# Optimization experiments

Measured on AMD Instinct MI355X. Metric: run time of the kernel, lower is better.

Reference implementation:

```python
import jax, jax.numpy as jnp
import numpy as np

N = 100000  # nodes
E = 600000  # edges
D = 128     # input_dim
H = D // 2  # hidden of MLP head
OUT = 10    # output_dim
EPS = 1e-5
NEG_SLOPE = 0.2


def _p(key, shape, scale):
    return jax.random.normal(key, shape, dtype=jnp.float32) * scale


def setup_inputs() -> dict:
    key = jax.random.key(0)
    ks = jax.random.split(key, 16)
    s = 1.0 / np.sqrt(D)
    return {
        "x": jax.random.normal(ks[0], (N, D), dtype=jnp.float32),
        "edge_index": jax.random.randint(ks[1], (2, E), 0, N, dtype=jnp.int64),
        # SAGEConv: lin_l (applied to mean-aggregated neighbors, has bias), lin_r (root)
        "sage_Wl": _p(ks[2], (D, D), s), "sage_Wr": _p(ks[3], (D, D), s),
        "sage_b": jnp.zeros((D,), jnp.float32),
        # GCNConv
        "gcn_W": _p(ks[4], (D, D), s), "gcn_b": jnp.zeros((D,), jnp.float32),
        # GATConv (heads=1)
        "gat_W": _p(ks[5], (D, D), s),
        "gat_att_src": _p(ks[6], (D,), s), "gat_att_dst": _p(ks[7], (D,), s),
        "gat_b": jnp.zeros((D,), jnp.float32),
        # BatchNorms (batch-stat normalization)
        "bn1_g": jnp.ones((D,), jnp.float32), "bn1_b": jnp.zeros((D,), jnp.float32),
        "bn2_g": jnp.ones((D,), jnp.float32), "bn2_b": jnp.zeros((D,), jnp.float32),
        "bn3_g": jnp.ones((D,), jnp.float32), "bn3_b": jnp.zeros((D,), jnp.float32),
        # MLP head
        "lin1_W": _p(ks[8], (D, H), s), "lin1_b": jnp.zeros((H,), jnp.float32),
        "lin2_W": _p(ks[9], (H, OUT), 1.0 / np.sqrt(H)), "lin2_b": jnp.zeros((OUT,), jnp.float32),
    }


def _bn_relu(x, g, b):
    mu = jnp.mean(x, axis=0)
    var = jnp.mean(jnp.square(x - mu), axis=0)
    return jax.nn.relu((x - mu) * jax.lax.rsqrt(var + EPS) * g + b)


def _sage(x, src, dst, Wl, Wr, b):
    agg = jax.ops.segment_sum(x[src], dst, num_segments=N)          # [N, D]
    cnt = jax.ops.segment_sum(jnp.ones((src.shape[0],), x.dtype), dst, num_segments=N)
    mean = agg / jnp.maximum(cnt, 1.0)[:, None]
    return mean @ Wl + x @ Wr + b


def _gcn(x, src, dst, W, b):
    loop = jnp.arange(N, dtype=src.dtype)
    s = jnp.concatenate([src, loop]); d = jnp.concatenate([dst, loop])
    deg = jax.ops.segment_sum(jnp.ones((d.shape[0],), x.dtype), d, num_segments=N)
    dinv = jnp.where(deg > 0, jax.lax.rsqrt(jnp.maximum(deg, 1.0)), 0.0)
    xw = x @ W
    msg = xw[s] * (dinv[s] * dinv[d])[:, None]
    return jax.ops.segment_sum(msg, d, num_segments=N) + b


def _gat(x, src, dst, W, att_s, att_d, b):
    loop = jnp.arange(N, dtype=src.dtype)
    s = jnp.concatenate([src, loop]); d = jnp.concatenate([dst, loop])
    xw = x @ W                                  # [N, D]
    a_s = xw @ att_s                            # [N]
    a_d = xw @ att_d                            # [N]
    e = jax.nn.leaky_relu(a_s[s] + a_d[d], NEG_SLOPE)  # [E+N]
    m = jax.ops.segment_max(e, d, num_segments=N)
    ee = jnp.exp(e - m[d])
    z = jax.ops.segment_sum(ee, d, num_segments=N)
    alpha = ee / z[d]
    return jax.ops.segment_sum(alpha[:, None] * xw[s], d, num_segments=N) + b


def reference(x, edge_index, sage_Wl, sage_Wr, sage_b, gcn_W, gcn_b,
              gat_W, gat_att_src, gat_att_dst, gat_b,
              bn1_g, bn1_b, bn2_g, bn2_b, bn3_g, bn3_b,
              lin1_W, lin1_b, lin2_W, lin2_b):
    src, dst = edge_index[0], edge_index[1]
    h = _bn_relu(_sage(x, src, dst, sage_Wl, sage_Wr, sage_b), bn1_g, bn1_b)
    h = _bn_relu(_gcn(h, src, dst, gcn_W, gcn_b), bn2_g, bn2_b)
    h = _bn_relu(_gat(h, src, dst, gat_W, gat_att_src, gat_att_dst, gat_b), bn3_g, bn3_b)
    # dropout is identity in eval mode
    h = jax.nn.relu(h @ lin1_W + lin1_b) @ lin2_W + lin2_b
    return jax.nn.log_softmax(h, axis=1)
```

## Files before the change

kernel.cpp:

```cpp
#include <hip/hip_runtime.h>

static constexpr int Dd = 128;
static constexpr int Hh = 64;
static constexpr int OC = 10;
#define CDIV(a,b) (((a)+(b)-1)/(b))

typedef __attribute__((ext_vector_type(8))) short short8v;
typedef __attribute__((ext_vector_type(16))) float f32x16;
typedef unsigned short u16;

__device__ __forceinline__ float lrelu(float x){ return x>0.f? x : 0.2f*x; }
__device__ __forceinline__ unsigned f2bf(float f){
  unsigned u = __float_as_uint(f);
  return (u + 0x7FFFu + ((u>>16)&1u)) >> 16;
}
__device__ __forceinline__ float bl(unsigned u){ return __uint_as_float(u<<16); }
__device__ __forceinline__ float bh(unsigned u){ return __uint_as_float(u & 0xFFFF0000u); }
__device__ __forceinline__ int swz(int byte, int row){ return byte ^ ((row&7)<<4); }

__global__ __launch_bounds__(256) void k_hist(const int* __restrict__ dst, int E,
    int* __restrict__ cnt) {
  int e = blockIdx.x*256 + threadIdx.x;
  if (e < E) atomicAdd(cnt + dst[e], 1);
}

__global__ __launch_bounds__(256) void k_scan_l1(const int* __restrict__ cnt,
    int* __restrict__ rp, int n, int* __restrict__ bsum) {
  __shared__ int sdata[256];
  int t = threadIdx.x;
  int base = blockIdx.x*2048 + t*8;
  int v[8]; int s = 0;
  #pragma unroll
  for (int k = 0; k < 8; k++) { v[k] = (base+k < n) ? cnt[base+k] : 0; s += v[k]; }
  sdata[t] = s; __syncthreads();
  for (int off = 1; off < 256; off <<= 1) {
    int a = sdata[t];
    int b = (t >= off) ? sdata[t-off] : 0;
    __syncthreads();
    sdata[t] = a + b;
    __syncthreads();
  }
  int ex = sdata[t] - s;
  if (t == 255) bsum[blockIdx.x] = sdata[255];
  int run = ex;
  #pragma unroll
  for (int k = 0; k < 8; k++) { if (base+k < n) rp[base+k] = run; run += v[k]; }
}

__global__ void k_scan_l2(int* __restrict__ bsum, int nb) {
  if (threadIdx.x == 0 && blockIdx.x == 0) {
    int run = 0;
    for (int i = 0; i < nb; i++) { int v = bsum[i]; bsum[i] = run; run += v; }
  }
}

__global__ __launch_bounds__(256) void k_scan_l3(int* __restrict__ rp, int n,
    const int* __restrict__ bsum, int E) {
  int off = bsum[blockIdx.x];
  int base = blockIdx.x*2048 + threadIdx.x*8;
  #pragma unroll
  for (int k = 0; k < 8; k++) if (base+k < n) rp[base+k] += off;
  if (blockIdx.x == 0 && threadIdx.x == 0) rp[n] = E;
}

__global__ __launch_bounds__(256) void k_fill(const int* __restrict__ src,
    const int* __restrict__ dst, int E, const int* __restrict__ rp,
    int* __restrict__ cnt, int* __restrict__ col) {
  int e = blockIdx.x*256 + threadIdx.x;
  if (e >= E) return;
  int d = dst[e];
  int pos = rp[d] + atomicSub(cnt + d, 1) - 1;
  col[pos] = src[e];
}

__global__ __launch_bounds__(256) void k_wt(const float* __restrict__ W,
    u16* __restrict__ WT, int K, int N) {
  int idx = blockIdx.x*256 + threadIdx.x;
  if (idx >= K*N) return;
  int n = idx / K, k = idx % K;
  WT[idx] = (u16)f2bf(W[k*N + n]);
}

__global__ __launch_bounds__(256) void k_tobf16(const float* __restrict__ in,
    u16* __restrict__ out, int n8) {
  int idx = blockIdx.x*256 + threadIdx.x;
  if (idx >= n8) return;
  const float4* p = reinterpret_cast<const float4*>(in) + idx*2;
  float4 v0 = p[0], v1 = p[1];
  uint4 w;
  w.x = f2bf(v0.x) | (f2bf(v0.y)<<16);
  w.y = f2bf(v0.z) | (f2bf(v0.w)<<16);
  w.z = f2bf(v1.x) | (f2bf(v1.y)<<16);
  w.w = f2bf(v1.z) | (f2bf(v1.w)<<16);
  reinterpret_cast<uint4*>(out)[idx] = w;
}

__global__ __launch_bounds__(256) void k_sage_gather(const u16* __restrict__ xb,
    const int* __restrict__ rp, const int* __restrict__ col,
    u16* __restrict__ ob, int n) {
  int gid = blockIdx.x*256 + threadIdx.x;
  int i = gid >> 5, l = gid & 31;
  if (i >= n) return;
  int beg = rp[i], end = rp[i+1];
  const u16* xp = xb + l*4;
  float a0=0.f, a1=0.f, a2=0.f, a3=0.f;
  int j = beg;
  for (; j+4 <= end; j += 4) {
    int s0=col[j], s1=col[j+1], s2=col[j+2], s3=col[j+3];
    uint2 v0 = *reinterpret_cast<const uint2*>(xp + (size_t)s0*Dd);
    uint2 v1 = *reinterpret_cast<const uint2*>(xp + (size_t)s1*Dd);
    uint2 v2 = *reinterpret_cast<const uint2*>(xp + (size_t)s2*Dd);
    uint2 v3 = *reinterpret_cast<const uint2*>(xp + (size_t)s3*Dd);
    a0 += (bl(v0.x)+bl(v1.x)) + (bl(v2.x)+bl(v3.x));
    a1 += (bh(v0.x)+bh(v1.x)) + (bh(v2.x)+bh(v3.x));
    a2 += (bl(v0.y)+bl(v1.y)) + (bl(v2.y)+bl(v3.y));
    a3 += (bh(v0.y)+bh(v1.y)) + (bh(v2.y)+bh(v3.y));
  }
  for (; j < end; j++) {
    int s = col[j];
    uint2 v = *reinterpret_cast<const uint2*>(xp + (size_t)s*Dd);
    a0 += bl(v.x); a1 += bh(v.x); a2 += bl(v.y); a3 += bh(v.y);
  }
  float inv = 1.0f / fmaxf((float)(end - beg), 1.0f);
  uint2 o;
  o.x = f2bf(a0*inv) | (f2bf(a1*inv)<<16);
  o.y = f2bf(a2*inv) | (f2bf(a3*inv)<<16);
  *reinterpret_cast<uint2*>(ob + (size_t)i*Dd + l*4) = o;
}

__global__ __launch_bounds__(256) void k_dinv(const int* __restrict__ rp,
    float* __restrict__ dinv, int n) {
  int i = blockIdx.x*256 + threadIdx.x;
  if (i < n) dinv[i] = rsqrtf((float)(rp[i+1] - rp[i]) + 1.0f);
}

__global__ __launch_bounds__(256) void k_gcn_gather(const u16* __restrict__ xb,
    const int* __restrict__ rp, const int* __restrict__ col,
    const float* __restrict__ dinv, u16* __restrict__ ob, int n) {
  int gid = blockIdx.x*256 + threadIdx.x;
  int i = gid >> 5, l = gid & 31;
  if (i >= n) return;
  int beg = rp[i], end = rp[i+1];
  const u16* xp = xb + l*4;
  float a0=0.f, a1=0.f, a2=0.f, a3=0.f;
  int j = beg;
  for (; j+4 <= end; j += 4) {
    int s0=col[j], s1=col[j+1], s2=col[j+2], s3=col[j+3];
    uint2 v0 = *reinterpret_cast<const uint2*>(xp + (size_t)s0*Dd);
    uint2 v1 = *reinterpret_cast<const uint2*>(xp + (size_t)s1*Dd);
    uint2 v2 = *reinterpret_cast<const uint2*>(xp + (size_t)s2*Dd);
    uint2 v3 = *reinterpret_cast<const uint2*>(xp + (size_t)s3*Dd);
    float w0 = dinv[s0], w1 = dinv[s1], w2 = dinv[s2], w3 = dinv[s3];
    a0 += (w0*bl(v0.x)+w1*bl(v1.x)) + (w2*bl(v2.x)+w3*bl(v3.x));
    a1 += (w0*bh(v0.x)+w1*bh(v1.x)) + (w2*bh(v2.x)+w3*bh(v3.x));
    a2 += (w0*bl(v0.y)+w1*bl(v1.y)) + (w2*bl(v2.y)+w3*bl(v3.y));
    a3 += (w0*bh(v0.y)+w1*bh(v1.y)) + (w2*bh(v2.y)+w3*bh(v3.y));
  }
  for (; j < end; j++) {
    int s = col[j];
    float w = dinv[s];
    uint2 v = *reinterpret_cast<const uint2*>(xp + (size_t)s*Dd);
    a0 += w*bl(v.x); a1 += w*bh(v.x); a2 += w*bl(v.y); a3 += w*bh(v.y);
  }
  float di = dinv[i];
  float ws = di*di;
  uint2 sv = *reinterpret_cast<const uint2*>(xp + (size_t)i*Dd);
  a0 = di*a0 + ws*bl(sv.x); a1 = di*a1 + ws*bh(sv.x);
  a2 = di*a2 + ws*bl(sv.y); a3 = di*a3 + ws*bh(sv.y);
  uint2 o;
  o.x = f2bf(a0) | (f2bf(a1)<<16);
  o.y = f2bf(a2) | (f2bf(a3)<<16);
  *reinterpret_cast<uint2*>(ob + (size_t)i*Dd + l*4) = o;
}

__global__ __launch_bounds__(256) void k_gat_gather(const u16* __restrict__ xb,
    const int* __restrict__ rp, const int* __restrict__ col,
    const float* __restrict__ a_s, const float* __restrict__ a_d,
    u16* __restrict__ ob, int n) {
  int gid = blockIdx.x*256 + threadIdx.x;
  int i = gid >> 5, l = gid & 31;
  if (i >= n) return;
  int beg = rp[i], end = rp[i+1];
  const u16* xp = xb + l*4;
  float ad = a_d[i];
  float es = lrelu(a_s[i] + ad);
  float m = es;
  int j = beg;
  for (; j+4 <= end; j += 4) {
    float e0 = lrelu(a_s[col[j]]   + ad);
    float e1 = lrelu(a_s[col[j+1]] + ad);
    float e2 = lrelu(a_s[col[j+2]] + ad);
    float e3 = lrelu(a_s[col[j+3]] + ad);
    m = fmaxf(m, fmaxf(fmaxf(e0,e1), fmaxf(e2,e3)));
  }
  for (; j < end; j++)
    m = fmaxf(m, lrelu(a_s[col[j]] + ad));
  float z = __expf(es - m);
  uint2 sv = *reinterpret_cast<const uint2*>(xp + (size_t)i*Dd);
  float a0 = z*bl(sv.x), a1 = z*bh(sv.x), a2 = z*bl(sv.y), a3 = z*bh(sv.y);
  j = beg;
  for (; j+4 <= end; j += 4) {
    int s0=col[j], s1=col[j+1], s2=col[j+2], s3=col[j+3];
    uint2 v0 = *reinterpret_cast<const uint2*>(xp + (size_t)s0*Dd);
    uint2 v1 = *reinterpret_cast<const uint2*>(xp + (size_t)s1*Dd);
    uint2 v2 = *reinterpret_cast<const uint2*>(xp + (size_t)s2*Dd);
    uint2 v3 = *reinterpret_cast<const uint2*>(xp + (size_t)s3*Dd);
    float w0 = __expf(lrelu(a_s[s0]+ad) - m);
    float w1 = __expf(lrelu(a_s[s1]+ad) - m);
    float w2 = __expf(lrelu(a_s[s2]+ad) - m);
    float w3 = __expf(lrelu(a_s[s3]+ad) - m);
    z += (w0+w1) + (w2+w3);
    a0 += (w0*bl(v0.x)+w1*bl(v1.x)) + (w2*bl(v2.x)+w3*bl(v3.x));
    a1 += (w0*bh(v0.x)+w1*bh(v1.x)) + (w2*bh(v2.x)+w3*bh(v3.x));
    a2 += (w0*bl(v0.y)+w1*bl(v1.y)) + (w2*bl(v2.y)+w3*bl(v3.y));
    a3 += (w0*bh(v0.y)+w1*bh(v1.y)) + (w2*bh(v2.y)+w3*bh(v3.y));
  }
  for (; j < end; j++) {
    int s = col[j];
    float w = __expf(lrelu(a_s[s]+ad) - m);
    z += w;
    uint2 v = *reinterpret_cast<const uint2*>(xp + (size_t)s*Dd);
    a0 += w*bl(v.x); a1 += w*bh(v.x); a2 += w*bl(v.y); a3 += w*bh(v.y);
  }
  float inv = 1.0f / z;
  uint2 o;
  o.x = f2bf(a0*inv) | (f2bf(a1*inv)<<16);
  o.y = f2bf(a2*inv) | (f2bf(a3*inv)<<16);
  *reinterpret_cast<uint2*>(ob + (size_t)i*Dd + l*4) = o;
}

__global__ __launch_bounds__(256) void k_bn_stats_bf(const u16* __restrict__ X, int M,
    float* __restrict__ gsum, float* __restrict__ gsq) {
  __shared__ float ss[2][256];
  int t = threadIdx.x;
  int cd = t & 63;
  int rg = t >> 6;
  float s0=0.f, q0=0.f, s1=0.f, q1=0.f;
  const unsigned* Xu = reinterpret_cast<const unsigned*>(X);
  for (int r = blockIdx.x*4 + rg; r < M; r += gridDim.x*4) {
    unsigned v = Xu[(size_t)r*64 + cd];
    float a = bl(v), b = bh(v);
    s0 += a; q0 += a*a; s1 += b; q1 += b*b;
  }
  ss[0][t] = s0; ss[1][t] = q0; __syncthreads();
  float rs0 = 0.f, rq0 = 0.f;
  if (rg == 0) {
    rs0 = ss[0][cd] + ss[0][cd+64] + ss[0][cd+128] + ss[0][cd+192];
    rq0 = ss[1][cd] + ss[1][cd+64] + ss[1][cd+128] + ss[1][cd+192];
  }
  __syncthreads();
  ss[0][t] = s1; ss[1][t] = q1; __syncthreads();
  if (rg == 0) {
    float rs1 = ss[0][cd] + ss[0][cd+64] + ss[0][cd+128] + ss[0][cd+192];
    float rq1 = ss[1][cd] + ss[1][cd+64] + ss[1][cd+128] + ss[1][cd+192];
    atomicAdd(gsum + 2*cd,     rs0); atomicAdd(gsq + 2*cd,     rq0);
    atomicAdd(gsum + 2*cd + 1, rs1); atomicAdd(gsq + 2*cd + 1, rq1);
  }
}

__global__ __launch_bounds__(128) void k_bn_final(const float* __restrict__ gsum,
    const float* __restrict__ gsq, int M, const float* __restrict__ g,
    const float* __restrict__ b, float* __restrict__ scale, float* __restrict__ shift) {
  int c = threadIdx.x;
  float mu = gsum[c] / (float)M;
  float var = fmaxf(gsq[c] / (float)M - mu*mu, 0.f);
  float sc = g[c] * rsqrtf(var + 1e-5f);
  scale[c] = sc;
  shift[c] = b[c] - mu*sc;
}

template<int NCOLS, bool DUAL, bool BNA, bool STATS, bool BIASRELU, bool ATT, bool OUTBF>
__global__ __launch_bounds__(256) void k_mm(
    const u16* __restrict__ A1, const u16* __restrict__ A2,
    const u16* __restrict__ WT1, const u16* __restrict__ WT2,
    const float* __restrict__ bnsc, const float* __restrict__ bnsh,
    const float* __restrict__ bias,
    void* __restrict__ Cout, int M,
    float* __restrict__ gsum, float* __restrict__ gsq,
    const float* __restrict__ att_sv, const float* __restrict__ att_dv,
    float* __restrict__ as_out, float* __restrict__ ad_out) {
  constexpr int NF = NCOLS/32;
  __shared__ char ldsA[128*128*2];
  __shared__ char ldsW[NCOLS*128*2];
  int t = threadIdx.x;
  int wave = t >> 6, l = t & 63;
  int lm = l & 31, h = l >> 5;
  int row0 = blockIdx.x*128;

  f32x16 acc[NF];
  #pragma unroll
  for (int nf = 0; nf < NF; nf++)
    #pragma unroll
    for (int i = 0; i < 16; i++) acc[nf][i] = 0.f;

  const int nph = DUAL ? 2 : 1;
  for (int ph = 0; ph < nph; ph++) {
    const u16* A = (DUAL && ph) ? A2 : A1;
    const u16* WT = (DUAL && ph) ? WT2 : WT1;
    #pragma unroll
    for (int i = 0; i < NCOLS*16/256; i++) {
      int c = i*256 + t; int nrow = c >> 4; int k0 = (c & 15) << 3;
      uint4 w = *reinterpret_cast<const uint4*>(WT + nrow*128 + k0);
      *reinterpret_cast<uint4*>(ldsW + swz(nrow*256 + k0*2, nrow)) = w;
    }
    #pragma unroll
    for (int i = 0; i < 8; i++) {
      int c = i*256 + t; int row = c >> 4; int k0 = (c & 15) << 3;
      uint4 w = {0,0,0,0};
      if (row0 + row < M)
        w = *reinterpret_cast<const uint4*>(A + (size_t)(row0+row)*128 + k0);
      if constexpr (BNA) {
        float4 sc0 = *reinterpret_cast<const float4*>(bnsc + k0);
        float4 sc1 = *reinterpret_cast<const float4*>(bnsc + k0 + 4);
        float4 sh0 = *reinterpret_cast<const float4*>(bnsh + k0);
        float4 sh1 = *reinterpret_cast<const float4*>(bnsh + k0 + 4);
        float e0 = fmaxf(bl(w.x)*sc0.x+sh0.x, 0.f), e1 = fmaxf(bh(w.x)*sc0.y+sh0.y, 0.f);
        float e2 = fmaxf(bl(w.y)*sc0.z+sh0.z, 0.f), e3 = fmaxf(bh(w.y)*sc0.w+sh0.w, 0.f);
        float e4 = fmaxf(bl(w.z)*sc1.x+sh1.x, 0.f), e5 = fmaxf(bh(w.z)*sc1.y+sh1.y, 0.f);
        float e6 = fmaxf(bl(w.w)*sc1.z+sh1.z, 0.f), e7 = fmaxf(bh(w.w)*sc1.w+sh1.w, 0.f);
        w.x = f2bf(e0) | (f2bf(e1)<<16);
        w.y = f2bf(e2) | (f2bf(e3)<<16);
        w.z = f2bf(e4) | (f2bf(e5)<<16);
        w.w = f2bf(e6) | (f2bf(e7)<<16);
      }
      *reinterpret_cast<uint4*>(ldsA + swz(row*256 + k0*2, row)) = w;
    }
    __syncthreads();
    #pragma unroll
    for (int ks = 0; ks < 8; ks++) {
      int kb = (ks*16 + h*8) * 2;
      int arow = wave*32 + lm;
      short8v af = *reinterpret_cast<short8v*>(ldsA + swz(arow*256 + kb, arow));
      #pragma unroll
      for (int nf = 0; nf < NF; nf++) {
        int brow = nf*32 + lm;
        short8v bf = *reinterpret_cast<short8v*>(ldsW + swz(brow*256 + kb, brow));
        acc[nf] = __builtin_amdgcn_mfma_f32_32x32x16_bf16(af, bf, acc[nf], 0, 0, 0);
      }
    }
    __syncthreads();
  }
  float* s_sum = reinterpret_cast<float*>(ldsW);
  float* s_sq  = s_sum + 128;
  if constexpr (STATS) {
    if (t < 128) { s_sum[t] = 0.f; s_sq[t] = 0.f; }
    __syncthreads();
  }
  #pragma unroll
  for (int nf = 0; nf < NF; nf++) {
    int colg = nf*32 + lm;
    float bv = 0.f;
    if constexpr (BIASRELU) bv = bias[colg];
    float ps = 0.f, pq = 0.f;
    #pragma unroll
    for (int reg = 0; reg < 16; reg++) {
      int row = row0 + wave*32 + (reg&3) + 8*(reg>>2) + 4*h;
      float v = acc[nf][reg];
      if constexpr (BIASRELU) v = fmaxf(v + bv, 0.f);
      if (row < M) {
        if constexpr (OUTBF)
          ((u16*)Cout)[(size_t)row*NCOLS + colg] = (u16)f2bf(v);
        else
          ((float*)Cout)[(size_t)row*NCOLS + colg] = v;
      }
      ps += v; pq += v*v;
    }
    if constexpr (STATS) {
      atomicAdd(&s_sum[colg], ps);
      atomicAdd(&s_sq[colg], pq);
    }
  }
  if constexpr (ATT) {
    float as_c[NF], ad_c[NF];
    #pragma unroll
    for (int nf = 0; nf < NF; nf++) { as_c[nf] = att_sv[nf*32+lm]; ad_c[nf] = att_dv[nf*32+lm]; }
    #pragma unroll
    for (int reg = 0; reg < 16; reg++) {
      float ps = 0.f, pd = 0.f;
      #pragma unroll
      for (int nf = 0; nf < NF; nf++) { float v = acc[nf][reg]; ps += v*as_c[nf]; pd += v*ad_c[nf]; }
      #pragma unroll
      for (int mm = 1; mm < 32; mm <<= 1) { ps += __shfl_xor(ps, mm); pd += __shfl_xor(pd, mm); }
      int row = row0 + wave*32 + (reg&3) + 8*(reg>>2) + 4*h;
      if (lm == 0 && row < M) { as_out[row] = ps; ad_out[row] = pd; }
    }
  }
  if constexpr (STATS) {
    __syncthreads();
    if (t < 128) { atomicAdd(gsum + t, s_sum[t]); atomicAdd(gsq + t, s_sq[t]); }
  }
}

__global__ __launch_bounds__(256) void k_head2(const float* __restrict__ M1,
    const float* __restrict__ W2, const float* __restrict__ b2,
    float* __restrict__ out, int n) {
  __shared__ float rows[256][65];
  __shared__ float w2s[Hh][OC];
  __shared__ float b2s[OC];
  int t = threadIdx.x;
  for (int i = t; i < Hh*OC; i += 256) w2s[i/OC][i%OC] = W2[i];
  if (t < OC) b2s[t] = b2[t];
  int r0 = blockIdx.x*256;
  #pragma unroll
  for (int i = 0; i < 16; i++) {
    int f = i*256 + t; int row = f >> 4; int c0 = (f & 15) << 2;
    float4 v = {0,0,0,0};
    if (r0 + row < n) v = *reinterpret_cast<const float4*>(M1 + (size_t)(r0+row)*Hh + c0);
    rows[row][c0+0] = v.x; rows[row][c0+1] = v.y;
    rows[row][c0+2] = v.z; rows[row][c0+3] = v.w;
  }
  __syncthreads();
  int row = r0 + t;
  if (row >= n) return;
  float p[OC];
  #pragma unroll
  for (int c = 0; c < OC; c++) p[c] = b2s[c];
  for (int k = 0; k < Hh; k++) {
    float a = rows[t][k];
    #pragma unroll
    for (int c = 0; c < OC; c++) p[c] += a * w2s[k][c];
  }
  float mx = p[0];
  #pragma unroll
  for (int c = 1; c < OC; c++) mx = fmaxf(mx, p[c]);
  float s = 0.f;
  #pragma unroll
  for (int c = 0; c < OC; c++) s += expf(p[c] - mx);
  float lse = mx + logf(s);
  #pragma unroll
  for (int c = 0; c < OC; c++) out[(size_t)row*OC + c] = p[c] - lse;
}

extern "C" void kernel_launch(void* const* d_in, const int* in_sizes, int n_in,
                              void* d_out, int out_size, void* d_ws, size_t ws_size,
                              hipStream_t stream) {
  const float* x       = (const float*)d_in[0];
  const int*   ei      = (const int*)d_in[1];
  const float* sage_Wl = (const float*)d_in[2];
  const float* sage_Wr = (const float*)d_in[3];
  const float* gcn_W   = (const float*)d_in[5];
  const float* gat_W   = (const float*)d_in[7];
  const float* att_s   = (const float*)d_in[8];
  const float* att_d   = (const float*)d_in[9];
  const float* bn1_g = (const float*)d_in[11], *bn1_b = (const float*)d_in[12];
  const float* bn2_g = (const float*)d_in[13], *bn2_b = (const float*)d_in[14];
  const float* bn3_g = (const float*)d_in[15], *bn3_b = (const float*)d_in[16];
  const float* lin1_W = (const float*)d_in[17], *lin1_b = (const float*)d_in[18];
  const float* lin2_W = (const float*)d_in[19], *lin2_b = (const float*)d_in[20];

  const int Nn = in_sizes[0] / Dd;
  const int Ee = in_sizes[1] / 2;
  const int* srcv = ei;
  const int* dstv = ei + Ee;

  u16* b0 = (u16*)d_ws;
  u16* b1 = b0 + (size_t)Nn*Dd;
  u16* b2 = b1 + (size_t)Nn*Dd;
  float* dinv  = (float*)(b2 + (size_t)Nn*Dd);
  float* a_s   = dinv + Nn;
  float* a_d   = a_s + Nn;
  float* bn_sum   = a_d + Nn;
  float* bn_sq    = bn_sum + Dd;
  float* bn_scale = bn_sq + Dd;
  float* bn_shift = bn_scale + Dd;
  int* rp    = (int*)(bn_shift + Dd);
  int* cnt_i = rp + (Nn + 1);
  int* bsum  = cnt_i + Nn;
  int* col   = bsum + 64;
  u16* wt_sWl = (u16*)(col + Ee);
  u16* wt_sWr = wt_sWl + 128*128;
  u16* wt_gcn = wt_sWr + 128*128;
  u16* wt_gat = wt_gcn + 128*128;
  u16* wt_l1  = wt_gat + 128*128;

  const dim3 B(256);
  const dim3 Gn(CDIV(Nn, 256));
  const dim3 Gn32(CDIV(Nn*32, 256));
  const dim3 Ge(CDIV(Ee, 256));
  const dim3 Gmm(CDIV(Nn, 128));
  const dim3 Ghead(CDIV(Nn, 256));
  const dim3 Gstat(512);
  const int nscan = CDIV(Nn, 2048);

  hipMemsetAsync(cnt_i, 0, (size_t)Nn*sizeof(int), stream);
  k_hist<<<Ge, B, 0, stream>>>(dstv, Ee, cnt_i);
  k_scan_l1<<<dim3(nscan), B, 0, stream>>>(cnt_i, rp, Nn, bsum);
  k_scan_l2<<<dim3(1), dim3(64), 0, stream>>>(bsum, nscan);
  k_scan_l3<<<dim3(nscan), B, 0, stream>>>(rp, Nn, bsum, Ee);
  k_fill<<<Ge, B, 0, stream>>>(srcv, dstv, Ee, rp, cnt_i, col);
  k_wt<<<dim3(64), B, 0, stream>>>(sage_Wl, wt_sWl, 128, 128);
  k_wt<<<dim3(64), B, 0, stream>>>(sage_Wr, wt_sWr, 128, 128);
  k_wt<<<dim3(64), B, 0, stream>>>(gcn_W,   wt_gcn, 128, 128);
  k_wt<<<dim3(64), B, 0, stream>>>(gat_W,   wt_gat, 128, 128);
  k_wt<<<dim3(32), B, 0, stream>>>(lin1_W,  wt_l1,  128, 64);
  k_tobf16<<<dim3(CDIV(Nn*Dd/8, 256)), B, 0, stream>>>(x, b0, Nn*Dd/8);
  k_dinv<<<Gn, B, 0, stream>>>(rp, dinv, Nn);

  k_sage_gather<<<Gn32, B, 0, stream>>>(b0, rp, col, b1, Nn);
  hipMemsetAsync(bn_sum, 0, 2*Dd*sizeof(float), stream);
  k_mm<128, true, false, true, false, false, true><<<Gmm, B, 0, stream>>>(
      b1, b0, wt_sWl, wt_sWr, nullptr, nullptr, nullptr, b2, Nn, bn_sum, bn_sq,
      nullptr, nullptr, nullptr, nullptr);
  k_bn_final<<<dim3(1), dim3(128), 0, stream>>>(bn_sum, bn_sq, Nn, bn1_g, bn1_b, bn_scale, bn_shift);

  k_mm<128, false, true, false, false, false, true><<<Gmm, B, 0, stream>>>(
      b2, nullptr, wt_gcn, nullptr, bn_scale, bn_shift, nullptr, b0, Nn, nullptr, nullptr,
      nullptr, nullptr, nullptr, nullptr);
  k_gcn_gather<<<Gn32, B, 0, stream>>>(b0, rp, col, dinv, b1, Nn);
  hipMemsetAsync(bn_sum, 0, 2*Dd*sizeof(float), stream);
  k_bn_stats_bf<<<Gstat, B, 0, stream>>>(b1, Nn, bn_sum, bn_sq);
  k_bn_final<<<dim3(1), dim3(128), 0, stream>>>(bn_sum, bn_sq, Nn, bn2_g, bn2_b, bn_scale, bn_shift);

  k_mm<128, false, true, false, false, true, true><<<Gmm, B, 0, stream>>>(
      b1, nullptr, wt_gat, nullptr, bn_scale, bn_shift, nullptr, b2, Nn, nullptr, nullptr,
      att_s, att_d, a_s, a_d);
  k_gat_gather<<<Gn32, B, 0, stream>>>(b2, rp, col, a_s, a_d, b0, Nn);
  hipMemsetAsync(bn_sum, 0, 2*Dd*sizeof(float), stream);
  k_bn_stats_bf<<<Gstat, B, 0, stream>>>(b0, Nn, bn_sum, bn_sq);
  k_bn_final<<<dim3(1), dim3(128), 0, stream>>>(bn_sum, bn_sq, Nn, bn3_g, bn3_b, bn_scale, bn_shift);

  float* m1 = (float*)b1;
  k_mm<64, false, true, false, true, false, false><<<Gmm, B, 0, stream>>>(
      b0, nullptr, wt_l1, nullptr, bn_scale, bn_shift, lin1_b, m1, Nn, nullptr, nullptr,
      nullptr, nullptr, nullptr, nullptr);
  k_head2<<<Ghead, B, 0, stream>>>(m1, lin2_W, lin2_b, (float*)d_out, Nn);
}
```

Measured before the change: 428.5 us.

## Sort nodes by degree, use online softmax in GAT, fuse BN-final into matmul

Adds a degree-bucket permutation so each gather kernel processes nodes of similar degree together, reducing divergence among warps with uneven neighbour counts. GAT gather switches to a single-pass online softmax instead of two passes over neighbours. BN finalisation is folded into the consuming matmul prologue, the five weight-transpose launches are merged into one, and the per-layer memsets are merged into one, cutting launch count. The permutation adds scattered writes to output rows and three small kernels, including a serial single-thread scan.

```diff
diff --git a/kernel.cpp b/kernel.cpp
--- a/kernel.cpp
+++ b/kernel.cpp
@@ -73,12 +73,49 @@
   col[pos] = src[e];
 }
 
-__global__ __launch_bounds__(256) void k_wt(const float* __restrict__ W,
-    u16* __restrict__ WT, int K, int N) {
+__global__ __launch_bounds__(256) void k_degprep(const int* __restrict__ rp, int n,
+    float* __restrict__ dinv, int* __restrict__ dcnt) {
+  int i = blockIdx.x*256 + threadIdx.x;
+  if (i >= n) return;
+  int deg = rp[i+1] - rp[i];
+  dinv[i] = rsqrtf((float)deg + 1.0f);
+  atomicAdd(&dcnt[deg > 63 ? 63 : deg], 1);
+}
+
+__global__ void k_degscan(const int* __restrict__ dcnt, int* __restrict__ dcur) {
+  if (threadIdx.x == 0 && blockIdx.x == 0) {
+    int run = 0;
+    for (int b = 0; b < 64; b++) { int v = dcnt[b]; dcur[b] = run; run += v; }
+  }
+}
+
+__global__ __launch_bounds__(256) void k_degfill(const int* __restrict__ rp, int n,
+    int* __restrict__ dcur, int* __restrict__ perm) {
+  int i = blockIdx.x*256 + threadIdx.x;
+  if (i >= n) return;
+  int deg = rp[i+1] - rp[i];
+  int pos = atomicAdd(&dcur[deg > 63 ? 63 : deg], 1);
+  perm[pos] = i;
+}
+
+__global__ __launch_bounds__(256) void k_wt_all(
+    const float* __restrict__ w0, const float* __restrict__ w1,
+    const float* __restrict__ w2, const float* __restrict__ w3,
+    const float* __restrict__ w4,
+    u16* __restrict__ o0, u16* __restrict__ o1, u16* __restrict__ o2,
+    u16* __restrict__ o3, u16* __restrict__ o4) {
   int idx = blockIdx.x*256 + threadIdx.x;
-  if (idx >= K*N) return;
-  int n = idx / K, k = idx % K;
-  WT[idx] = (u16)f2bf(W[k*N + n]);
+  const float* W; u16* O; int base, N;
+  if (idx < 65536) {
+    int m = idx >> 14;
+    W = m==0?w0 : m==1?w1 : m==2?w2 : w3;
+    O = m==0?o0 : m==1?o1 : m==2?o2 : o3;
+    base = idx & 16383; N = 128;
+  } else if (idx < 73728) {
+    W = w4; O = o4; base = idx - 65536; N = 64;
+  } else return;
+  int n = base / 128, k = base % 128;
+  O[base] = (u16)f2bf(W[k*N + n]);
 }
 
 __global__ __launch_bounds__(256) void k_tobf16(const float* __restrict__ in,
@@ -97,10 +134,11 @@
 
 __global__ __launch_bounds__(256) void k_sage_gather(const u16* __restrict__ xb,
     const int* __restrict__ rp, const int* __restrict__ col,
-    u16* __restrict__ ob, int n) {
+    const int* __restrict__ perm, u16* __restrict__ ob, int n) {
   int gid = blockIdx.x*256 + threadIdx.x;
-  int i = gid >> 5, l = gid & 31;
-  if (i >= n) return;
+  int g = gid >> 5, l = gid & 31;
+  if (g >= n) return;
+  int i = perm[g];
   int beg = rp[i], end = rp[i+1];
   const u16* xp = xb + l*4;
   float a0=0.f, a1=0.f, a2=0.f, a3=0.f;
@@ -128,18 +166,14 @@
   *reinterpret_cast<uint2*>(ob + (size_t)i*Dd + l*4) = o;
 }
 
-__global__ __launch_bounds__(256) void k_dinv(const int* __restrict__ rp,
-    float* __restrict__ dinv, int n) {
-  int i = blockIdx.x*256 + threadIdx.x;
-  if (i < n) dinv[i] = rsqrtf((float)(rp[i+1] - rp[i]) + 1.0f);
-}
-
 __global__ __launch_bounds__(256) void k_gcn_gather(const u16* __restrict__ xb,
     const int* __restrict__ rp, const int* __restrict__ col,
-    const float* __restrict__ dinv, u16* __restrict__ ob, int n) {
+    const int* __restrict__ perm, const float* __restrict__ dinv,
+    u16* __restrict__ ob, int n) {
   int gid = blockIdx.x*256 + threadIdx.x;
-  int i = gid >> 5, l = gid & 31;
-  if (i >= n) return;
+  int g = gid >> 5, l = gid & 31;
+  if (g >= n) return;
+  int i = perm[g];
   int beg = rp[i], end = rp[i+1];
   const u16* xp = xb + l*4;
   float a0=0.f, a1=0.f, a2=0.f, a3=0.f;
@@ -175,40 +209,37 @@
 
 __global__ __launch_bounds__(256) void k_gat_gather(const u16* __restrict__ xb,
     const int* __restrict__ rp, const int* __restrict__ col,
+    const int* __restrict__ perm,
     const float* __restrict__ a_s, const float* __restrict__ a_d,
     u16* __restrict__ ob, int n) {
   int gid = blockIdx.x*256 + threadIdx.x;
-  int i = gid >> 5, l = gid & 31;
-  if (i >= n) return;
+  int g = gid >> 5, l = gid & 31;
+  if (g >= n) return;
+  int i = perm[g];
   int beg = rp[i], end = rp[i+1];
   const u16* xp = xb + l*4;
   float ad = a_d[i];
-  float es = lrelu(a_s[i] + ad);
-  float m = es;
+  float m = lrelu(a_s[i] + ad);
+  float z = 1.0f;
+  uint2 sv = *reinterpret_cast<const uint2*>(xp + (size_t)i*Dd);
+  float a0 = bl(sv.x), a1 = bh(sv.x), a2 = bl(sv.y), a3 = bh(sv.y);
   int j = beg;
-  for (; j+4 <= end; j += 4) {
-    float e0 = lrelu(a_s[col[j]]   + ad);
-    float e1 = lrelu(a_s[col[j+1]] + ad);
-    float e2 = lrelu(a_s[col[j+2]] + ad);
-    float e3 = lrelu(a_s[col[j+3]] + ad);
-    m = fmaxf(m, fmaxf(fmaxf(e0,e1), fmaxf(e2,e3)));
-  }
-  for (; j < end; j++)
-    m = fmaxf(m, lrelu(a_s[col[j]] + ad));
-  float z = __expf(es - m);
-  uint2 sv = *reinterpret_cast<const uint2*>(xp + (size_t)i*Dd);
-  float a0 = z*bl(sv.x), a1 = z*bh(sv.x), a2 = z*bl(sv.y), a3 = z*bh(sv.y);
-  j = beg;
   for (; j+4 <= end; j += 4) {
     int s0=col[j], s1=col[j+1], s2=col[j+2], s3=col[j+3];
     uint2 v0 = *reinterpret_cast<const uint2*>(xp + (size_t)s0*Dd);
     uint2 v1 = *reinterpret_cast<const uint2*>(xp + (size_t)s1*Dd);
     uint2 v2 = *reinterpret_cast<const uint2*>(xp + (size_t)s2*Dd);
     uint2 v3 = *reinterpret_cast<const uint2*>(xp + (size_t)s3*Dd);
-    float w0 = __expf(lrelu(a_s[s0]+ad) - m);
-    float w1 = __expf(lrelu(a_s[s1]+ad) - m);
-    float w2 = __expf(lrelu(a_s[s2]+ad) - m);
-    float w3 = __expf(lrelu(a_s[s3]+ad) - m);
+    float e0 = lrelu(a_s[s0]+ad), e1 = lrelu(a_s[s1]+ad);
+    float e2 = lrelu(a_s[s2]+ad), e3 = lrelu(a_s[s3]+ad);
+    float mg = fmaxf(fmaxf(e0,e1), fmaxf(e2,e3));
+    if (mg > m) {
+      float r = __expf(m - mg);
+      z *= r; a0 *= r; a1 *= r; a2 *= r; a3 *= r;
+      m = mg;
+    }
+    float w0 = __expf(e0-m), w1 = __expf(e1-m);
+    float w2 = __expf(e2-m), w3 = __expf(e3-m);
     z += (w0+w1) + (w2+w3);
     a0 += (w0*bl(v0.x)+w1*bl(v1.x)) + (w2*bl(v2.x)+w3*bl(v3.x));
     a1 += (w0*bh(v0.x)+w1*bh(v1.x)) + (w2*bh(v2.x)+w3*bh(v3.x));
@@ -217,9 +248,15 @@
   }
   for (; j < end; j++) {
     int s = col[j];
-    float w = __expf(lrelu(a_s[s]+ad) - m);
+    uint2 v = *reinterpret_cast<const uint2*>(xp + (size_t)s*Dd);
+    float e = lrelu(a_s[s]+ad);
+    if (e > m) {
+      float r = __expf(m - e);
+      z *= r; a0 *= r; a1 *= r; a2 *= r; a3 *= r;
+      m = e;
+    }
+    float w = __expf(e-m);
     z += w;
-    uint2 v = *reinterpret_cast<const uint2*>(xp + (size_t)s*Dd);
     a0 += w*bl(v.x); a1 += w*bh(v.x); a2 += w*bl(v.y); a3 += w*bh(v.y);
   }
   float inv = 1.0f / z;
@@ -258,22 +295,12 @@
   }
 }
 
-__global__ __launch_bounds__(128) void k_bn_final(const float* __restrict__ gsum,
-    const float* __restrict__ gsq, int M, const float* __restrict__ g,
-    const float* __restrict__ b, float* __restrict__ scale, float* __restrict__ shift) {
-  int c = threadIdx.x;
-  float mu = gsum[c] / (float)M;
-  float var = fmaxf(gsq[c] / (float)M - mu*mu, 0.f);
-  float sc = g[c] * rsqrtf(var + 1e-5f);
-  scale[c] = sc;
-  shift[c] = b[c] - mu*sc;
-}
-
 template<int NCOLS, bool DUAL, bool BNA, bool STATS, bool BIASRELU, bool ATT, bool OUTBF>
 __global__ __launch_bounds__(256) void k_mm(
     const u16* __restrict__ A1, const u16* __restrict__ A2,
     const u16* __restrict__ WT1, const u16* __restrict__ WT2,
-    const float* __restrict__ bnsc, const float* __restrict__ bnsh,
+    const float* __restrict__ bng, const float* __restrict__ bnb,
+    const float* __restrict__ bsum_in, const float* __restrict__ bsq_in,
     const float* __restrict__ bias,
     void* __restrict__ Cout, int M,
     float* __restrict__ gsum, float* __restrict__ gsq,
@@ -282,10 +309,22 @@
   constexpr int NF = NCOLS/32;
   __shared__ char ldsA[128*128*2];
   __shared__ char ldsW[NCOLS*128*2];
+  __shared__ float s_scale[128], s_shift[128];
   int t = threadIdx.x;
   int wave = t >> 6, l = t & 63;
   int lm = l & 31, h = l >> 5;
   int row0 = blockIdx.x*128;
+
+  if constexpr (BNA) {
+    if (t < 128) {
+      float mu = bsum_in[t] / (float)M;
+      float var = fmaxf(bsq_in[t] / (float)M - mu*mu, 0.f);
+      float sc = bng[t] * rsqrtf(var + 1e-5f);
+      s_scale[t] = sc;
+      s_shift[t] = bnb[t] - mu*sc;
+    }
+    __syncthreads();
+  }
 
   f32x16 acc[NF];
   #pragma unroll
@@ -310,10 +349,10 @@
       if (row0 + row < M)
         w = *reinterpret_cast<const uint4*>(A + (size_t)(row0+row)*128 + k0);
       if constexpr (BNA) {
-        float4 sc0 = *reinterpret_cast<const float4*>(bnsc + k0);
-        float4 sc1 = *reinterpret_cast<const float4*>(bnsc + k0 + 4);
-        float4 sh0 = *reinterpret_cast<const float4*>(bnsh + k0);
-        float4 sh1 = *reinterpret_cast<const float4*>(bnsh + k0 + 4);
+        float4 sc0 = *reinterpret_cast<const float4*>(&s_scale[k0]);
+        float4 sc1 = *reinterpret_cast<const float4*>(&s_scale[k0+4]);
+        float4 sh0 = *reinterpret_cast<const float4*>(&s_shift[k0]);
+        float4 sh1 = *reinterpret_cast<const float4*>(&s_shift[k0+4]);
         float e0 = fmaxf(bl(w.x)*sc0.x+sh0.x, 0.f), e1 = fmaxf(bh(w.x)*sc0.y+sh0.y, 0.f);
         float e2 = fmaxf(bl(w.y)*sc0.z+sh0.z, 0.f), e3 = fmaxf(bh(w.y)*sc0.w+sh0.w, 0.f);
         float e4 = fmaxf(bl(w.z)*sc1.x+sh1.x, 0.f), e5 = fmaxf(bh(w.z)*sc1.y+sh1.y, 0.f);
@@ -459,14 +498,17 @@
   float* dinv  = (float*)(b2 + (size_t)Nn*Dd);
   float* a_s   = dinv + Nn;
   float* a_d   = a_s + Nn;
-  float* bn_sum   = a_d + Nn;
-  float* bn_sq    = bn_sum + Dd;
-  float* bn_scale = bn_sq + Dd;
-  float* bn_shift = bn_scale + Dd;
-  int* rp    = (int*)(bn_shift + Dd);
+  float* bs    = a_d + Nn;
+  float* bs1_sum = bs,        *bs1_sq = bs + 128;
+  float* bs2_sum = bs + 256,  *bs2_sq = bs + 384;
+  float* bs3_sum = bs + 512,  *bs3_sq = bs + 640;
+  int* rp    = (int*)(bs + 768);
   int* cnt_i = rp + (Nn + 1);
   int* bsum  = cnt_i + Nn;
-  int* col   = bsum + 64;
+  int* dcnt  = bsum + 64;
+  int* dcur  = dcnt + 64;
+  int* perm  = dcur + 64;
+  int* col   = perm + Nn;
   u16* wt_sWl = (u16*)(col + Ee);
   u16* wt_sWr = wt_sWl + 128*128;
   u16* wt_gcn = wt_sWr + 128*128;
@@ -483,45 +525,41 @@
   const int nscan = CDIV(Nn, 2048);
 
   hipMemsetAsync(cnt_i, 0, (size_t)Nn*sizeof(int), stream);
+  hipMemsetAsync(dcnt, 0, 64*sizeof(int), stream);
+  hipMemsetAsync(bs, 0, 768*sizeof(float), stream);
+
   k_hist<<<Ge, B, 0, stream>>>(dstv, Ee, cnt_i);
   k_scan_l1<<<dim3(nscan), B, 0, stream>>>(cnt_i, rp, Nn, bsum);
   k_scan_l2<<<dim3(1), dim3(64), 0, stream>>>(bsum, nscan);
   k_scan_l3<<<dim3(nscan), B, 0, stream>>>(rp, Nn, bsum, Ee);
   k_fill<<<Ge, B, 0, stream>>>(srcv, dstv, Ee, rp, cnt_i, col);
-  k_wt<<<dim3(64), B, 0, stream>>>(sage_Wl, wt_sWl, 128, 128);
-  k_wt<<<dim3(64), B, 0, stream>>>(sage_Wr, wt_sWr, 128, 128);
-  k_wt<<<dim3(64), B, 0, stream>>>(gcn_W,   wt_gcn, 128, 128);
-  k_wt<<<dim3(64), B, 0, stream>>>(gat_W,   wt_gat, 128, 128);
-  k_wt<<<dim3(32), B, 0, stream>>>(lin1_W,  wt_l1,  128, 64);
+  k_degprep<<<Gn, B, 0, stream>>>(rp, Nn, dinv, dcnt);
+  k_degscan<<<dim3(1), dim3(64), 0, stream>>>(dcnt, dcur);
+  k_degfill<<<Gn, B, 0, stream>>>(rp, Nn, dcur, perm);
+  k_wt_all<<<dim3(288), B, 0, stream>>>(sage_Wl, sage_Wr, gcn_W, gat_W, lin1_W,
+                                        wt_sWl, wt_sWr, wt_gcn, wt_gat, wt_l1);
   k_tobf16<<<dim3(CDIV(Nn*Dd/8, 256)), B, 0, stream>>>(x, b0, Nn*Dd/8);
-  k_dinv<<<Gn, B, 0, stream>>>(rp, dinv, Nn);
-
-  k_sage_gather<<<Gn32, B, 0, stream>>>(b0, rp, col, b1, Nn);
-  hipMemsetAsync(bn_sum, 0, 2*Dd*sizeof(float), stream);
+
+  k_sage_gather<<<Gn32, B, 0, stream>>>(b0, rp, col, perm, b1, Nn);
   k_mm<128, true, false, true, false, false, true><<<Gmm, B, 0, stream>>>(
-      b1, b0, wt_sWl, wt_sWr, nullptr, nullptr, nullptr, b2, Nn, bn_sum, bn_sq,
-      nullptr, nullptr, nullptr, nullptr);
-  k_bn_final<<<dim3(1), dim3(128), 0, stream>>>(bn_sum, bn_sq, Nn, bn1_g, bn1_b, bn_scale, bn_shift);
+      b1, b0, wt_sWl, wt_sWr, nullptr, nullptr, nullptr, nullptr, nullptr,
+      b2, Nn, bs1_sum, bs1_sq, nullptr, nullptr, nullptr, nullptr);
 
   k_mm<128, false, true, false, false, false, true><<<Gmm, B, 0, stream>>>(
-      b2, nullptr, wt_gcn, nullptr, bn_scale, bn_shift, nullptr, b0, Nn, nullptr, nullptr,
-      nullptr, nullptr, nullptr, nullptr);
-  k_gcn_gather<<<Gn32, B, 0, stream>>>(b0, rp, col, dinv, b1, Nn);
-  hipMemsetAsync(bn_sum, 0, 2*Dd*sizeof(float), stream);
-  k_bn_stats_bf<<<Gstat, B, 0, stream>>>(b1, Nn, bn_sum, bn_sq);
-  k_bn_final<<<dim3(1), dim3(128), 0, stream>>>(bn_sum, bn_sq, Nn, bn2_g, bn2_b, bn_scale, bn_shift);
+      b2, nullptr, wt_gcn, nullptr, bn1_g, bn1_b, bs1_sum, bs1_sq, nullptr,
+      b0, Nn, nullptr, nullptr, nullptr, nullptr, nullptr, nullptr);
+  k_gcn_gather<<<Gn32, B, 0, stream>>>(b0, rp, col, perm, dinv, b1, Nn);
+  k_bn_stats_bf<<<Gstat, B, 0, stream>>>(b1, Nn, bs2_sum, bs2_sq);
 
   k_mm<128, false, true, false, false, true, true><<<Gmm, B, 0, stream>>>(
-      b1, nullptr, wt_gat, nullptr, bn_scale, bn_shift, nullptr, b2, Nn, nullptr, nullptr,
-      att_s, att_d, a_s, a_d);
-  k_gat_gather<<<Gn32, B, 0, stream>>>(b2, rp, col, a_s, a_d, b0, Nn);
-  hipMemsetAsync(bn_sum, 0, 2*Dd*sizeof(float), stream);
-  k_bn_stats_bf<<<Gstat, B, 0, stream>>>(b0, Nn, bn_sum, bn_sq);
-  k_bn_final<<<dim3(1), dim3(128), 0, stream>>>(bn_sum, bn_sq, Nn, bn3_g, bn3_b, bn_scale, bn_shift);
+      b1, nullptr, wt_gat, nullptr, bn2_g, bn2_b, bs2_sum, bs2_sq, nullptr,
+      b2, Nn, nullptr, nullptr, att_s, att_d, a_s, a_d);
+  k_gat_gather<<<Gn32, B, 0, stream>>>(b2, rp, col, perm, a_s, a_d, b0, Nn);
+  k_bn_stats_bf<<<Gstat, B, 0, stream>>>(b0, Nn, bs3_sum, bs3_sq);
 
   float* m1 = (float*)b1;
   k_mm<64, false, true, false, true, false, false><<<Gmm, B, 0, stream>>>(
-      b0, nullptr, wt_l1, nullptr, bn_scale, bn_shift, lin1_b, m1, Nn, nullptr, nullptr,
-      nullptr, nullptr, nullptr, nullptr);
+      b0, nullptr, wt_l1, nullptr, bn3_g, bn3_b, bs3_sum, bs3_sq, lin1_b,
+      m1, Nn, nullptr, nullptr, nullptr, nullptr, nullptr, nullptr);
   k_head2<<<Ghead, B, 0, stream>>>(m1, lin2_W, lin2_b, (float*)d_out, Nn);
 }
```

New measurement: 1.134 ms. 2.65x slower.
